# Kernel tuning notes

Hardware: AMD Instinct MI355X
Metric: run time of the kernel (lower is better)

## Reference

```python
import jax, jax.numpy as jnp
import numpy as np

B, T, N_EMBED, HEAD_SIZE = 8, 2048, 1024, 64


def setup_inputs() -> dict:
    key = jax.random.key(0)
    kx, kq, kk, kv = jax.random.split(key, 4)
    x = jax.random.normal(kx, (B, T, N_EMBED), dtype=jnp.float32)
    # nn.Linear(n_embed, head_size, bias=False) -> weight [head_size, n_embed];
    # we store the transposed [n_embed, head_size] so projection is x @ W.
    s = 1.0 / np.sqrt(N_EMBED)
    Wq = jax.random.normal(kq, (N_EMBED, HEAD_SIZE), dtype=jnp.float32) * s
    Wk = jax.random.normal(kk, (N_EMBED, HEAD_SIZE), dtype=jnp.float32) * s
    Wv = jax.random.normal(kv, (N_EMBED, HEAD_SIZE), dtype=jnp.float32) * s
    pad_mask = jnp.ones((B, T), dtype=jnp.int32)
    return {"x": x, "pad_mask": pad_mask, "Wq": Wq, "Wk": Wk, "Wv": Wv}


def reference(x, pad_mask, Wq, Wk, Wv):
    Bq, Tq, C = x.shape  # C == n_embed
    q = x @ Wq  # [B,T,H]
    k = x @ Wk  # self-attention path (enc_x is None)
    v = x @ Wv
    # NOTE: original divides by C**0.5 with C = n_embed, not head_size.
    scores = jnp.einsum("bth,bsh->bts", q, k) / jnp.sqrt(jnp.asarray(C, x.dtype))
    causal = jnp.tril(jnp.ones((Tq, Tq), dtype=bool))  # tril[:T,:T] != 0
    keep = causal[None, :, :] & (pad_mask[:, None, :] != 0)  # [B,T,T]
    scores = jnp.where(keep, scores, -jnp.inf)
    attn = jax.nn.softmax(scores, axis=-1)
    return jnp.einsum("bts,bsh->bth", attn, v)  # [B,T,head_size]
```

## Files before the change

kernel.cpp:

```cpp
#include <hip/hip_runtime.h>

#define DEV static __device__ __forceinline__

typedef float f32x4 __attribute__((ext_vector_type(4)));
typedef int i32x4 __attribute__((ext_vector_type(4)));
typedef __bf16 bf16x8 __attribute__((ext_vector_type(8)));
typedef unsigned short u16x8 __attribute__((ext_vector_type(8)));
typedef unsigned short u16x4 __attribute__((ext_vector_type(4)));

#define MFMA(a, b, c) __builtin_amdgcn_mfma_f32_16x16x32_bf16((a), (b), (c), 0, 0, 0)

#define WAIT8_BARRIER() asm volatile("s_waitcnt vmcnt(8)\n\ts_barrier" ::: "memory")
#define WAIT4_BARRIER() asm volatile("s_waitcnt vmcnt(4)\n\ts_barrier" ::: "memory")
#define LGKM_BARRIER()  asm volatile("s_waitcnt lgkmcnt(0)\n\ts_barrier" ::: "memory")
#define VM_DRAIN()      asm volatile("s_waitcnt vmcnt(0)" ::: "memory")

#define TT 2048
#define CE 1024
#define HS 64

#define WBT_E 0
#define Q_E   196608
#define K_E   (Q_E + 1048576)
#define VT_E  (K_E + 1048576)
#define PO_E  (VT_E + 1048576)
#define PML_E (PO_E + 2097152)

DEV unsigned short cvt_bf16(float f) {
    unsigned int u = __builtin_bit_cast(unsigned int, f);
    u += 0x7FFFu + ((u >> 16) & 1u);
    return (unsigned short)(u >> 16);
}

DEV float bf2f(unsigned short v) {
    unsigned int u = ((unsigned int)v) << 16;
    return __builtin_bit_cast(float, u);
}

DEV bf16x8 ld_bf8(const unsigned short* p) {
    union { u16x8 u; bf16x8 b; } v;
    v.u = *(const u16x8*)p;
    return v.b;
}

DEV bf16x8 as_bf8(u16x8 u) {
    union { u16x8 u; bf16x8 b; } v;
    v.u = u;
    return v.b;
}

DEV void glds16(const void* g, void* l) {
    __builtin_amdgcn_global_load_lds(
        (const __attribute__((address_space(1))) void*)g,
        (__attribute__((address_space(3))) void*)l, 16, 0, 0);
}

__global__ __launch_bounds__(256) void wconv_kernel(
        const float* __restrict__ Wq, const float* __restrict__ Wk,
        const float* __restrict__ Wv, unsigned short* __restrict__ wbt) {
    __shared__ unsigned short Tr[64 * 72];
    const int blk = blockIdx.x;
    const int head = blk >> 4, kt = blk & 15;
    const int k0 = kt * 64;
    const float* W = (head == 0) ? Wq : ((head == 1) ? Wk : Wv);
    const float sc = (head == 0) ? 0.045084220027780106f : 1.0f;
    const int t = threadIdx.x;
    const int rrow = t >> 4, c4 = (t & 15) * 4;
    for (int i = 0; i < 4; ++i) {
        int krow = rrow + i * 16;
        f32x4 f = *(const f32x4*)(W + (size_t)(k0 + krow) * 64 + c4);
        Tr[(c4 + 0) * 72 + krow] = cvt_bf16(f[0] * sc);
        Tr[(c4 + 1) * 72 + krow] = cvt_bf16(f[1] * sc);
        Tr[(c4 + 2) * 72 + krow] = cvt_bf16(f[2] * sc);
        Tr[(c4 + 3) * 72 + krow] = cvt_bf16(f[3] * sc);
    }
    __syncthreads();
    const int n = t >> 2, off = (t & 3) * 16;
    u16x8 a0 = *(const u16x8*)&Tr[n * 72 + off];
    u16x8 a1 = *(const u16x8*)&Tr[n * 72 + off + 8];
    unsigned short* dst = wbt + head * 65536 + n * 1024 + k0 + off;
    *(u16x8*)dst = a0;
    *(u16x8*)(dst + 8) = a1;
}

__global__ __launch_bounds__(512, 4) void proj_kernel(
        const float* __restrict__ x, const unsigned short* __restrict__ wbt,
        unsigned short* __restrict__ qws, unsigned short* __restrict__ kws,
        unsigned short* __restrict__ vtws) {
    __shared__ __align__(16) float Xt0[1024], Xt1[1024], Xt2[1024], Xt3[1024];
    __shared__ __align__(16) unsigned short Wt0[6144], Wt1[6144], Wt2[6144], Wt3[6144];
    __shared__ __align__(16) unsigned short TT2[64 * 48];

    const int t = threadIdx.x;
    const int lane = t & 63, w = t >> 6;
    const int quad = lane >> 4, c = lane & 15;
    const int wm = w & 1, wn = w >> 1;
    const int t0 = blockIdx.x * 32;

    const int srow = lane >> 3, scb = (lane & 7) ^ srow;
    const int wrow = lane >> 2, wcb = (lane & 3) ^ (wrow & 3);
    const int xrow = (w < 2) ? (t0 + w * 16 + srow) : t0;
    const int wbase = (w < 2) ? 0 : (w - 2) * 32;
    const float* xg0 = x + (size_t)xrow * CE + scb * 4;
    const float* xg1 = xg0 + (size_t)8 * CE;
    const unsigned short* wg0 = wbt + (size_t)(wbase + wrow) * 1024 + wcb * 8;
    const unsigned short* wg1 = wg0 + (size_t)16 * 1024;

#define PSTAGE(XD, WD, ksn) \
    if (w < 2) { \
        glds16(xg0 + (ksn), &XD[w * 512]); \
        glds16(xg1 + (ksn), &XD[w * 512 + 256]); \
    } else { \
        glds16(wg0 + (ksn), &WD[wbase * 32]); \
        glds16(wg1 + (ksn), &WD[wbase * 32 + 512]); \
    }

    f32x4 acc[3] = {};

    PSTAGE(Xt0, Wt0, 0)
    PSTAGE(Xt1, Wt1, 32)
    PSTAGE(Xt2, Wt2, 64)

    const int r32 = (wm * 16 + c) * 32;
    const int ck7 = c & 7, ck3 = c & 3;

#define PITER(step, XT, WT, XD, WD) { \
    WAIT4_BARRIER(); \
    f32x4 v0 = *(const f32x4*)&XT[r32 + (((2 * quad) ^ ck7) * 4)]; \
    f32x4 v1 = *(const f32x4*)&XT[r32 + (((2 * quad + 1) ^ ck7) * 4)]; \
    u16x8 ap; \
    _Pragma("unroll") for (int j = 0; j < 4; ++j) { \
        ap[j] = cvt_bf16(v0[j]); ap[4 + j] = cvt_bf16(v1[j]); } \
    bf16x8 af = as_bf8(ap); \
    _Pragma("unroll") for (int nt = 0; nt < 3; ++nt) { \
        bf16x8 bb = ld_bf8(&WT[(wn * 48 + nt * 16 + c) * 32 + ((quad ^ ck3) * 8)]); \
        acc[nt] = MFMA(af, bb, acc[nt]); } \
    const int ksn = (((step) + 3) & 31) * 32; \
    PSTAGE(XD, WD, ksn) }

    for (int s = 0; s < 32; s += 4) {
        PITER(s + 0, Xt0, Wt0, Xt3, Wt3)
        PITER(s + 1, Xt1, Wt1, Xt0, Wt0)
        PITER(s + 2, Xt2, Wt2, Xt1, Wt1)
        PITER(s + 3, Xt3, Wt3, Xt2, Wt2)
    }
#undef PITER
#undef PSTAGE

#pragma unroll
    for (int nt = 0; nt < 3; ++nt) {
        int col = wn * 48 + nt * 16 + c;
        f32x4 a = acc[nt];
#pragma unroll
        for (int r4 = 0; r4 < 4; ++r4) {
            int row = wm * 16 + quad * 4 + r4;
            size_t tg = (size_t)(t0 + row);
            unsigned short hv = cvt_bf16(a[r4]);
            if (col < 64)       qws[tg * HS + col] = hv;
            else if (col < 128) kws[tg * HS + col - 64] = hv;
            else                TT2[(col - 128) * 48 + row] = hv;
        }
    }
    __syncthreads();
    if (t < 256) {
        int h = t >> 2, off = (t & 3) * 8;
        u16x8 v = *(const u16x8*)&TT2[h * 48 + off];
        int b = t0 >> 11, tl0 = t0 & 2047;
        *(u16x8*)(vtws + (size_t)(b * 64 + h) * TT + tl0 + off) = v;
    }
}

__global__ __launch_bounds__(256) void flash_kernel(
        const unsigned short* __restrict__ qws, const unsigned short* __restrict__ kws,
        const unsigned short* __restrict__ vtws, const int* __restrict__ pmask,
        unsigned short* __restrict__ pO, float* __restrict__ pml) {
    __shared__ __align__(16) unsigned short Kt0[4096], Kt1[4096], Kt2[4096], Kt3[4096];
    __shared__ __align__(16) unsigned short Vt0[4096], Vt1[4096], Vt2[4096], Vt3[4096];
    __shared__ __align__(16) unsigned short Ps[4][1152];
    __shared__ __align__(16) float Bs[1024];

    const int t = threadIdx.x, blk = blockIdx.x;
    const int sp = blk >> 8, r8 = blk & 255, b = r8 & 7;
    int qt = r8 >> 3;
    if (sp) qt = 31 - qt;
    if (sp && qt == 0) return;
    const int half = (qt + 2) >> 1;
    const int jbeg = sp ? half : 0;
    const int jend = sp ? qt + 1 : half;
    const int niter = jend - jbeg;

    const int lane = t & 63, w = t >> 6;
    const int quad = lane >> 4, c = lane & 15;

    const int srow = lane >> 3, scb = (lane & 7) ^ srow;
    const unsigned short* kg0 = kws + (size_t)(b * TT + 2 * w * 8 + srow) * HS + scb * 8;
    const unsigned short* kg1 = kg0 + (size_t)8 * HS;
    const unsigned short* vg0 = vtws + (size_t)(b * 64 + 2 * w * 8 + srow) * TT + scb * 8;
    const unsigned short* vg1 = vg0 + (size_t)8 * TT;

#define FSTAGE(KD, VD, kv) \
    glds16(kg0 + (size_t)(kv) * HS, &KD[(2 * w + 0) * 512]); \
    glds16(kg1 + (size_t)(kv) * HS, &KD[(2 * w + 1) * 512]); \
    glds16(vg0 + (kv), &VD[(2 * w + 0) * 512]); \
    glds16(vg1 + (kv), &VD[(2 * w + 1) * 512]);

    bf16x8 qf[2];
#pragma unroll
    for (int kk = 0; kk < 2; ++kk)
        qf[kk] = ld_bf8(qws + (size_t)(b * TT + qt * 64 + w * 16 + c) * HS + kk * 32 + quad * 8);

    {
        int bi = t * 4;
        if (bi < niter * 64) {
            i32x4 pmv = *(const i32x4*)(pmask + b * TT + jbeg * 64 + bi);
            f32x4 bvv;
#pragma unroll
            for (int j = 0; j < 4; ++j) bvv[j] = pmv[j] ? 0.0f : -1e30f;
            *(f32x4*)&Bs[bi] = bvv;
        }
    }

    {
        int j1 = (jbeg + 1 > jend - 1) ? jend - 1 : jbeg + 1;
        int j2 = (jbeg + 2 > jend - 1) ? jend - 1 : jbeg + 2;
        FSTAGE(Kt0, Vt0, jbeg * 64)
        FSTAGE(Kt1, Vt1, j1 * 64)
        FSTAGE(Kt2, Vt2, j2 * 64)
    }
    LGKM_BARRIER();

    f32x4 o[4] = {};
    float m_run = -1e30f, l_run = 0.0f;
    const int ck7 = c & 7;

#define FITER(u, KT, VT, KD, VD) \
    if (j0 + (u) < jend) { \
        const int j = j0 + (u); \
        WAIT8_BARRIER(); \
        f32x4 bv[4]; \
        _Pragma("unroll") for (int nt = 0; nt < 4; ++nt) \
            bv[nt] = *(const f32x4*)&Bs[(j - jbeg) * 64 + nt * 16 + quad * 4]; \
        f32x4 s4[4] = {}; \
        _Pragma("unroll") for (int kk = 0; kk < 2; ++kk) \
        _Pragma("unroll") for (int nt = 0; nt < 4; ++nt) { \
            bf16x8 ka = ld_bf8(&KT[(nt * 16 + c) * 64 + (((kk * 4 + quad) ^ ck7) * 8)]); \
            s4[nt] = MFMA(ka, qf[kk], s4[nt]); } \
        if (j == qt) { \
            const int qrl = w * 16 + c; \
            _Pragma("unroll") for (int nt = 0; nt < 4; ++nt) \
            _Pragma("unroll") for (int r = 0; r < 4; ++r) { \
                int kvl = nt * 16 + quad * 4 + r; \
                s4[nt][r] = (kvl > qrl) ? -1e30f : (s4[nt][r] + bv[nt][r]); } \
        } else { \
            _Pragma("unroll") for (int nt = 0; nt < 4; ++nt) \
            _Pragma("unroll") for (int r = 0; r < 4; ++r) s4[nt][r] += bv[nt][r]; } \
        float mx = s4[0][0]; \
        _Pragma("unroll") for (int nt = 0; nt < 4; ++nt) \
        _Pragma("unroll") for (int r = 0; r < 4; ++r) mx = fmaxf(mx, s4[nt][r]); \
        mx = fmaxf(mx, __shfl_xor(mx, 16, 64)); \
        mx = fmaxf(mx, __shfl_xor(mx, 32, 64)); \
        float mnew = fmaxf(m_run, mx); \
        float al = exp2f(m_run - mnew); \
        m_run = mnew; \
        _Pragma("unroll") for (int nt = 0; nt < 4; ++nt) \
        _Pragma("unroll") for (int r = 0; r < 4; ++r) s4[nt][r] = exp2f(s4[nt][r] - mnew); \
        float rs = 0.0f; \
        _Pragma("unroll") for (int nt = 0; nt < 4; ++nt) \
            rs += (s4[nt][0] + s4[nt][1]) + (s4[nt][2] + s4[nt][3]); \
        rs += __shfl_xor(rs, 16, 64); \
        rs += __shfl_xor(rs, 32, 64); \
        l_run = l_run * al + rs; \
        _Pragma("unroll") for (int ht = 0; ht < 4; ++ht) \
        _Pragma("unroll") for (int r = 0; r < 4; ++r) o[ht][r] *= al; \
        _Pragma("unroll") for (int nt = 0; nt < 4; ++nt) { \
            u16x4 pk; \
            _Pragma("unroll") for (int r = 0; r < 4; ++r) pk[r] = cvt_bf16(s4[nt][r]); \
            *(u16x4*)&Ps[w][c * 72 + nt * 16 + quad * 4] = pk; } \
        bf16x8 p0 = ld_bf8(&Ps[w][c * 72 + quad * 8]); \
        bf16x8 p1 = ld_bf8(&Ps[w][c * 72 + 32 + quad * 8]); \
        _Pragma("unroll") for (int kk = 0; kk < 2; ++kk) { \
            bf16x8 pa = kk ? p1 : p0; \
            _Pragma("unroll") for (int ht = 0; ht < 4; ++ht) { \
                bf16x8 va = ld_bf8(&VT[(ht * 16 + c) * 64 + (((kk * 4 + quad) ^ ck7) * 8)]); \
                o[ht] = MFMA(va, pa, o[ht]); } } \
        int jn = j + 3; if (jn > jend - 1) jn = jend - 1; \
        FSTAGE(KD, VD, jn * 64) \
    }

    for (int j0 = jbeg; j0 < jend; j0 += 4) {
        FITER(0, Kt0, Vt0, Kt3, Vt3)
        FITER(1, Kt1, Vt1, Kt0, Vt0)
        FITER(2, Kt2, Vt2, Kt1, Vt1)
        FITER(3, Kt3, Vt3, Kt2, Vt2)
    }
#undef FITER
#undef FSTAGE

    VM_DRAIN();

    unsigned short* po = pO + (size_t)blk * 4096;
#pragma unroll
    for (int ht = 0; ht < 4; ++ht) {
        u16x4 pk;
#pragma unroll
        for (int r = 0; r < 4; ++r) pk[r] = cvt_bf16(o[ht][r]);
        *(u16x4*)(po + (w * 16 + c) * 64 + ht * 16 + quad * 4) = pk;
    }
    if (quad == 0) {
        pml[(size_t)blk * 128 + (w * 16 + c) * 2] = m_run;
        pml[(size_t)blk * 128 + (w * 16 + c) * 2 + 1] = l_run;
    }
}

__global__ __launch_bounds__(256) void combine_kernel(
        const unsigned short* __restrict__ pO, const float* __restrict__ pml,
        float* __restrict__ out) {
    const int blk = blockIdx.x;
    const int qt = blk >> 3, b = blk & 7;
    const int s0 = qt * 8 + b, s1 = 256 + (31 - qt) * 8 + b;
    const bool two = (qt > 0);
    const int t = threadIdx.x, h = t & 63, rg = t >> 6;
    for (int i = 0; i < 16; ++i) {
        int row = rg + i * 4;
        float m0 = pml[(size_t)s0 * 128 + row * 2];
        float l0 = pml[(size_t)s0 * 128 + row * 2 + 1];
        float o0 = bf2f(pO[(size_t)s0 * 4096 + row * 64 + h]);
        float num, den;
        if (two) {
            float m1 = pml[(size_t)s1 * 128 + row * 2];
            float l1 = pml[(size_t)s1 * 128 + row * 2 + 1];
            float o1 = bf2f(pO[(size_t)s1 * 4096 + row * 64 + h]);
            float M = fmaxf(m0, m1);
            float w0 = exp2f(m0 - M), w1 = exp2f(m1 - M);
            num = o0 * w0 + o1 * w1;
            den = l0 * w0 + l1 * w1;
        } else {
            num = o0; den = l0;
        }
        out[(size_t)(b * TT + qt * 64 + row) * HS + h] = num / den;
    }
}

extern "C" void kernel_launch(void* const* d_in, const int* in_sizes, int n_in,
                              void* d_out, int out_size, void* d_ws, size_t ws_size,
                              hipStream_t stream) {
    const float* x  = (const float*)d_in[0];
    const int* pm   = (const int*)d_in[1];
    const float* Wq = (const float*)d_in[2];
    const float* Wk = (const float*)d_in[3];
    const float* Wv = (const float*)d_in[4];
    float* out = (float*)d_out;

    unsigned short* wsu  = (unsigned short*)d_ws;
    unsigned short* wbt  = wsu + WBT_E;
    unsigned short* qws  = wsu + Q_E;
    unsigned short* kws  = wsu + K_E;
    unsigned short* vtws = wsu + VT_E;
    unsigned short* pO   = wsu + PO_E;
    float* pml           = (float*)(wsu + PML_E);

    wconv_kernel<<<48, 256, 0, stream>>>(Wq, Wk, Wv, wbt);
    proj_kernel<<<512, 512, 0, stream>>>(x, wbt, qws, kws, vtws);
    flash_kernel<<<512, 256, 0, stream>>>(qws, kws, vtws, pm, pO, pml);
    combine_kernel<<<256, 256, 0, stream>>>(pO, pml, out);
}
```

Before: 162.0 us.

## Enlarge projection tile to 64 rows and 64-wide k-steps with 3-stage pipeline

The projection kernel now processes 64 tokens per block with 64-element k slices, each wave computing two row fragments against three column fragments. This halves the number of blocks and the redundant loads of the weight tile per token, improving MFMA-to-load ratio. The pipeline drops from four to three LDS buffers with larger stages, increasing LDS use and lowering occupancy (launch bounds 2 blocks).

New measurement: 147.5 us. -9.0%, faster.

```diff
diff --git a/kernel.cpp b/kernel.cpp
--- a/kernel.cpp
+++ b/kernel.cpp
@@ -11,7 +11,7 @@
 #define MFMA(a, b, c) __builtin_amdgcn_mfma_f32_16x16x32_bf16((a), (b), (c), 0, 0, 0)
 
 #define WAIT8_BARRIER() asm volatile("s_waitcnt vmcnt(8)\n\ts_barrier" ::: "memory")
-#define WAIT4_BARRIER() asm volatile("s_waitcnt vmcnt(4)\n\ts_barrier" ::: "memory")
+#define WAIT5_BARRIER() asm volatile("s_waitcnt vmcnt(5)\n\ts_barrier" ::: "memory")
 #define LGKM_BARRIER()  asm volatile("s_waitcnt lgkmcnt(0)\n\ts_barrier" ::: "memory")
 #define VM_DRAIN()      asm volatile("s_waitcnt vmcnt(0)" ::: "memory")
 
@@ -83,88 +83,98 @@
     *(u16x8*)(dst + 8) = a1;
 }
 
-__global__ __launch_bounds__(512, 4) void proj_kernel(
+__global__ __launch_bounds__(512, 2) void proj_kernel(
         const float* __restrict__ x, const unsigned short* __restrict__ wbt,
         unsigned short* __restrict__ qws, unsigned short* __restrict__ kws,
         unsigned short* __restrict__ vtws) {
-    __shared__ __align__(16) float Xt0[1024], Xt1[1024], Xt2[1024], Xt3[1024];
-    __shared__ __align__(16) unsigned short Wt0[6144], Wt1[6144], Wt2[6144], Wt3[6144];
-    __shared__ __align__(16) unsigned short TT2[64 * 48];
+    __shared__ __align__(16) float Xt0[4096], Xt1[4096], Xt2[4096];
+    __shared__ __align__(16) unsigned short Wt0[12288], Wt1[12288], Wt2[12288];
+    __shared__ __align__(16) unsigned short TT2[64 * 72];
 
     const int t = threadIdx.x;
     const int lane = t & 63, w = t >> 6;
     const int quad = lane >> 4, c = lane & 15;
     const int wm = w & 1, wn = w >> 1;
-    const int t0 = blockIdx.x * 32;
-
-    const int srow = lane >> 3, scb = (lane & 7) ^ srow;
-    const int wrow = lane >> 2, wcb = (lane & 3) ^ (wrow & 3);
-    const int xrow = (w < 2) ? (t0 + w * 16 + srow) : t0;
-    const int wbase = (w < 2) ? 0 : (w - 2) * 32;
-    const float* xg0 = x + (size_t)xrow * CE + scb * 4;
-    const float* xg1 = xg0 + (size_t)8 * CE;
-    const unsigned short* wg0 = wbt + (size_t)(wbase + wrow) * 1024 + wcb * 8;
-    const unsigned short* wg1 = wg0 + (size_t)16 * 1024;
-
-#define PSTAGE(XD, WD, ksn) \
-    if (w < 2) { \
-        glds16(xg0 + (ksn), &XD[w * 512]); \
-        glds16(xg1 + (ksn), &XD[w * 512 + 256]); \
-    } else { \
-        glds16(wg0 + (ksn), &WD[wbase * 32]); \
-        glds16(wg1 + (ksn), &WD[wbase * 32 + 512]); \
-    }
-
-    f32x4 acc[3] = {};
+    const int t0 = blockIdx.x * 64;
+    const int ck7 = c & 7;
+
+    const int sxr = lane >> 4;
+    const int sxc0 = (lane & 15) ^ sxr;
+    const int sxc1 = (lane & 15) ^ ((4 + sxr) & 7);
+    const float* xg0 = x + (size_t)(t0 + w * 8 + 0 + sxr) * CE + sxc0 * 4;
+    const float* xg1 = x + (size_t)(t0 + w * 8 + 4 + sxr) * CE + sxc1 * 4;
+    const int swc = lane >> 3;
+    const int swk = (lane & 7) ^ swc;
+    const unsigned short* wg0 = wbt + (size_t)(w * 24 + 0 + swc) * 1024 + swk * 8;
+    const unsigned short* wg1 = wbt + (size_t)(w * 24 + 8 + swc) * 1024 + swk * 8;
+    const unsigned short* wg2 = wbt + (size_t)(w * 24 + 16 + swc) * 1024 + swk * 8;
+
+#define PSTAGE(XD, WD, ks) { \
+    const int kf = (ks) * 64; \
+    glds16(xg0 + kf, &XD[(w * 8 + 0) * 64]); \
+    glds16(xg1 + kf, &XD[(w * 8 + 4) * 64]); \
+    glds16(wg0 + kf, &WD[(w * 24 + 0) * 64]); \
+    glds16(wg1 + kf, &WD[(w * 24 + 8) * 64]); \
+    glds16(wg2 + kf, &WD[(w * 24 + 16) * 64]); }
+
+    f32x4 acc[2][3] = {};
 
     PSTAGE(Xt0, Wt0, 0)
-    PSTAGE(Xt1, Wt1, 32)
-    PSTAGE(Xt2, Wt2, 64)
-
-    const int r32 = (wm * 16 + c) * 32;
-    const int ck7 = c & 7, ck3 = c & 3;
+    PSTAGE(Xt1, Wt1, 1)
 
 #define PITER(step, XT, WT, XD, WD) { \
-    WAIT4_BARRIER(); \
-    f32x4 v0 = *(const f32x4*)&XT[r32 + (((2 * quad) ^ ck7) * 4)]; \
-    f32x4 v1 = *(const f32x4*)&XT[r32 + (((2 * quad + 1) ^ ck7) * 4)]; \
-    u16x8 ap; \
-    _Pragma("unroll") for (int j = 0; j < 4; ++j) { \
-        ap[j] = cvt_bf16(v0[j]); ap[4 + j] = cvt_bf16(v1[j]); } \
-    bf16x8 af = as_bf8(ap); \
-    _Pragma("unroll") for (int nt = 0; nt < 3; ++nt) { \
-        bf16x8 bb = ld_bf8(&WT[(wn * 48 + nt * 16 + c) * 32 + ((quad ^ ck3) * 8)]); \
-        acc[nt] = MFMA(af, bb, acc[nt]); } \
-    const int ksn = (((step) + 3) & 31) * 32; \
-    PSTAGE(XD, WD, ksn) }
-
-    for (int s = 0; s < 32; s += 4) {
-        PITER(s + 0, Xt0, Wt0, Xt3, Wt3)
+    WAIT5_BARRIER(); \
+    bf16x8 af[2][2]; \
+    _Pragma("unroll") for (int rf = 0; rf < 2; ++rf) \
+    _Pragma("unroll") for (int kk = 0; kk < 2; ++kk) { \
+        const int row = wm * 32 + rf * 16 + c; \
+        const int lc = kk * 8 + quad * 2; \
+        f32x4 v0 = *(const f32x4*)&XT[row * 64 + ((lc ^ ck7) * 4)]; \
+        f32x4 v1 = *(const f32x4*)&XT[row * 64 + (((lc + 1) ^ ck7) * 4)]; \
+        u16x8 ap; \
+        _Pragma("unroll") for (int j = 0; j < 4; ++j) { \
+            ap[j] = cvt_bf16(v0[j]); ap[4 + j] = cvt_bf16(v1[j]); } \
+        af[rf][kk] = as_bf8(ap); \
+    } \
+    _Pragma("unroll") for (int nt = 0; nt < 3; ++nt) \
+    _Pragma("unroll") for (int kk = 0; kk < 2; ++kk) { \
+        const int col = wn * 48 + nt * 16 + c; \
+        bf16x8 bb = ld_bf8(&WT[col * 64 + (((kk * 4 + quad) ^ ck7) * 8)]); \
+        acc[0][nt] = MFMA(af[0][kk], bb, acc[0][nt]); \
+        acc[1][nt] = MFMA(af[1][kk], bb, acc[1][nt]); \
+    } \
+    PSTAGE(XD, WD, (((step) + 2) & 15)) }
+
+    for (int s = 0; s < 15; s += 3) {
+        PITER(s + 0, Xt0, Wt0, Xt2, Wt2)
         PITER(s + 1, Xt1, Wt1, Xt0, Wt0)
         PITER(s + 2, Xt2, Wt2, Xt1, Wt1)
-        PITER(s + 3, Xt3, Wt3, Xt2, Wt2)
-    }
+    }
+    PITER(15, Xt0, Wt0, Xt2, Wt2)
 #undef PITER
 #undef PSTAGE
 
 #pragma unroll
-    for (int nt = 0; nt < 3; ++nt) {
-        int col = wn * 48 + nt * 16 + c;
-        f32x4 a = acc[nt];
-#pragma unroll
-        for (int r4 = 0; r4 < 4; ++r4) {
-            int row = wm * 16 + quad * 4 + r4;
-            size_t tg = (size_t)(t0 + row);
-            unsigned short hv = cvt_bf16(a[r4]);
-            if (col < 64)       qws[tg * HS + col] = hv;
-            else if (col < 128) kws[tg * HS + col - 64] = hv;
-            else                TT2[(col - 128) * 48 + row] = hv;
+    for (int rf = 0; rf < 2; ++rf) {
+#pragma unroll
+        for (int nt = 0; nt < 3; ++nt) {
+            int col = wn * 48 + nt * 16 + c;
+            f32x4 a = acc[rf][nt];
+#pragma unroll
+            for (int r4 = 0; r4 < 4; ++r4) {
+                int row = wm * 32 + rf * 16 + quad * 4 + r4;
+                size_t tg = (size_t)(t0 + row);
+                unsigned short hv = cvt_bf16(a[r4]);
+                if (col < 64)       qws[tg * HS + col] = hv;
+                else if (col < 128) kws[tg * HS + col - 64] = hv;
+                else                TT2[(col - 128) * 72 + row] = hv;
+            }
         }
     }
     __syncthreads();
-    if (t < 256) {
-        int h = t >> 2, off = (t & 3) * 8;
-        u16x8 v = *(const u16x8*)&TT2[h * 48 + off];
+    {
+        int h = t >> 3, off = (t & 7) * 8;
+        u16x8 v = *(const u16x8*)&TT2[h * 72 + off];
         int b = t0 >> 11, tl0 = t0 & 2047;
         *(u16x8*)(vtws + (size_t)(b * 64 + h) * TT + tl0 + off) = v;
     }
@@ -360,7 +370,7 @@
     float* pml           = (float*)(wsu + PML_E);
 
     wconv_kernel<<<48, 256, 0, stream>>>(Wq, Wk, Wv, wbt);
-    proj_kernel<<<512, 512, 0, stream>>>(x, wbt, qws, kws, vtws);
+    proj_kernel<<<256, 512, 0, stream>>>(x, wbt, qws, kws, vtws);
     flash_kernel<<<512, 256, 0, stream>>>(qws, kws, vtws, pm, pO, pml);
     combine_kernel<<<256, 256, 0, stream>>>(pO, pml, out);
 }
```
